# Kernel optimization log

Measured on AMD Instinct MI355X. Metric: run time of the kernel, lower is better.

The kernel has to match this reference:

```python
import jax, jax.numpy as jnp
import numpy as np
import math

B, S, D, H = 2, 2048, 512, 8  # batch, seq, d_hidden (= per-head dim here), n_heads


def _rope(x):
    # x: [B, H, S, D]; standard interleaved RoPE with base 10000
    b, h, s, d = x.shape
    inv_freq = 1.0 / (10000.0 ** (jnp.arange(0, d, 2, dtype=jnp.float32) / d))  # [d/2]
    ang = jnp.arange(s, dtype=jnp.float32)[:, None] * inv_freq[None, :]          # [S, d/2]
    cos, sin = jnp.cos(ang), jnp.sin(ang)
    x1, x2 = x[..., 0::2], x[..., 1::2]
    r1 = x1 * cos - x2 * sin
    r2 = x1 * sin + x2 * cos
    return jnp.stack([r1, r2], axis=-1).reshape(b, h, s, d).astype(x.dtype)


def setup_inputs() -> dict:
    key = jax.random.key(0)
    kq, k1, k2, k3, k4 = jax.random.split(key, 5)
    std = 0.02
    return {
        "q": jax.random.normal(kq, (B, S, D), dtype=jnp.float32),
        "W_q": jax.random.normal(k1, (H, D, D), dtype=jnp.float32) * std,
        "W_k": jax.random.normal(k2, (H, D, D), dtype=jnp.float32) * std,
        "W_v": jax.random.normal(k3, (H, D, D), dtype=jnp.float32) * std,
        "W_o": jax.random.normal(k4, (H * D, D), dtype=jnp.float32) * std,
    }


def reference(q, W_q, W_k, W_v, W_o):
    b, s, d = q.shape
    h = W_q.shape[0]
    scale = 1.0 / math.sqrt(d)
    qh = jnp.einsum('bsz,hzd->bhsd', q, W_q)
    kh = jnp.einsum('bsz,hzd->bhsd', q, W_k)
    vh = jnp.einsum('bsz,hzd->bhsd', q, W_v)
    qh = _rope(qh)
    kh = _rope(kh)
    scores = jnp.einsum('bhqd,bhkd->bhqk', qh, kh) * scale
    causal = jnp.triu(jnp.ones((s, s), dtype=bool), k=1)  # True above diagonal
    scores = jnp.where(causal, -jnp.inf, scores)
    probs = jax.nn.softmax(scores, axis=-1)  # dropout is identity in eval
    # NOTE: faithful to the original (transposed) einsum: contracts over the
    # query index z of probs with the sequence index z of v.
    out = jnp.einsum('bhzs,bhzd->bhsd', probs, vh)
    out = out.transpose(0, 2, 1, 3).reshape(b, s, h * d)
    return jnp.einsum('bsz,zd->bsd', out, W_o)
```

## Files before the change

kernel.cpp:

```cpp
#include <hip/hip_runtime.h>
#include <hip/hip_bf16.h>
#include <math.h>
#include <stdint.h>

#define BB 2
#define SS 2048
#define DD 512
#define HH 8
#define NTOK (BB*SS)
#define NQKV (3*HH*DD)
#define BHD  (HH*DD)
#define NBH  (BB*HH)
#define NTILE 136

typedef __attribute__((ext_vector_type(8))) short short8v;
typedef __attribute__((ext_vector_type(4))) float floatx4;

__device__ __forceinline__ unsigned short f2bf(float f) {
  unsigned int u = __builtin_bit_cast(unsigned int, f);
  u = (u + 0x7FFFu + ((u >> 16) & 1u)) >> 16;
  return (unsigned short)u;
}
__device__ __forceinline__ float bf2f(unsigned short s) {
  unsigned int u = ((unsigned int)s) << 16;
  return __builtin_bit_cast(float, u);
}
__device__ __forceinline__ void async16(const void* g, void* l) {
  __builtin_amdgcn_global_load_lds(
      (const __attribute__((address_space(1))) unsigned int*)g,
      (__attribute__((address_space(3))) unsigned int*)l, 16, 0, 0);
}

__global__ void k_convert_q(const float* __restrict__ q, unsigned short* __restrict__ qbf) {
  int i = (blockIdx.x * 256 + threadIdx.x) * 4;
  const float4 v = *(const float4*)&q[i];
  ushort4 o;
  o.x = f2bf(v.x); o.y = f2bf(v.y); o.z = f2bf(v.z); o.w = f2bf(v.w);
  *(ushort4*)&qbf[i] = o;
}

__global__ void k_rope_tab(float* __restrict__ rope) {
  const int idx = blockIdx.x * 256 + threadIdx.x;
  const int dp = idx >> 11, s = idx & 2047;
  const float inv = exp2f(-13.287712379549449f * (1.0f/256.0f) * (float)dp);
  float sn, cs;
  __sincosf((float)s * inv, &sn, &cs);
  rope[(size_t)idx * 2]     = cs;
  rope[(size_t)idx * 2 + 1] = sn;
}

__global__ void k_prep_w(const float* __restrict__ Wq, const float* __restrict__ Wk,
                         const float* __restrict__ Wv, const float* __restrict__ Wo,
                         unsigned short* __restrict__ Wcat, unsigned short* __restrict__ Wot) {
  __shared__ float t[32][33];
  const int z = blockIdx.z;
  const float* in; unsigned short* out; int inLD, outLD;
  float sc = 1.0f;
  if (z < 24) {
    int tsel = z / 8, h = z % 8;
    const float* w = (tsel == 0) ? Wq : (tsel == 1) ? Wk : Wv;
    if (tsel == 0) sc = 0.044194173824159216f;
    in = w + (size_t)h * DD * DD;
    out = Wcat + ((size_t)tsel * BHD + (size_t)h * DD) * DD;
    inLD = DD; outLD = DD;
  } else {
    int k = z - 24;
    in = Wo + (size_t)k * DD * DD;
    out = Wot + (size_t)k * DD;
    inLD = DD; outLD = BHD;
  }
  const int tx = threadIdx.x, ty = threadIdx.y;
  const int bx = blockIdx.x * 32, by = blockIdx.y * 32;
  for (int kk = 0; kk < 4; ++kk)
    t[ty + 8*kk][tx] = in[(size_t)(by + ty + 8*kk) * inLD + bx + tx];
  __syncthreads();
  for (int kk = 0; kk < 4; ++kk)
    out[(size_t)(bx + ty + 8*kk) * outLD + by + tx] = f2bf(t[tx][ty + 8*kk] * sc);
}

__global__ __launch_bounds__(256, 2)
void k_qkv(const unsigned short* __restrict__ Abf, const unsigned short* __restrict__ Bt,
           const float* __restrict__ rope,
           unsigned short* __restrict__ Qr, unsigned short* __restrict__ Kr,
           unsigned short* __restrict__ Vt) {
  __shared__ short As[128*32];
  __shared__ short Bs[256*32];
  const int tid = threadIdx.x;
  const int m0 = blockIdx.x * 128;
  const int n0 = blockIdx.y * 256;
  const int wave = tid >> 6, lane = tid & 63, qd = lane >> 4, c = lane & 15;
  const int wm = (wave >> 1) * 64, wn = (wave & 1) * 128;
  floatx4 acc[4][8] = {};
  const int e0 = tid * 8;
  const int r0 = e0 >> 5, c0 = e0 & 31;
  for (int k0 = 0; k0 < 512; k0 += 32) {
    __syncthreads();
    async16(&Abf[(size_t)(m0 + r0      ) * 512 + k0 + c0], &As[e0]);
    async16(&Abf[(size_t)(m0 + r0 +  64) * 512 + k0 + c0], &As[e0 + 2048]);
    async16(&Bt [(size_t)(n0 + r0      ) * 512 + k0 + c0], &Bs[e0]);
    async16(&Bt [(size_t)(n0 + r0 +  64) * 512 + k0 + c0], &Bs[e0 + 2048]);
    async16(&Bt [(size_t)(n0 + r0 + 128) * 512 + k0 + c0], &Bs[e0 + 4096]);
    async16(&Bt [(size_t)(n0 + r0 + 192) * 512 + k0 + c0], &Bs[e0 + 6144]);
    __syncthreads();
    short8v a[4], bfr[8];
    for (int mt = 0; mt < 4; ++mt) a[mt]   = *(const short8v*)&As[(wm + mt*16 + c)*32 + qd*8];
    for (int nt = 0; nt < 8; ++nt) bfr[nt] = *(const short8v*)&Bs[(wn + nt*16 + c)*32 + qd*8];
    for (int mt = 0; mt < 4; ++mt)
      for (int nt = 0; nt < 8; ++nt)
        acc[mt][nt] = __builtin_amdgcn_mfma_f32_16x16x32_bf16(a[mt], bfr[nt], acc[mt][nt], 0, 0, 0);
  }
  const int tsel = n0 >> 12;
  const int h = (n0 >> 9) & 7;
  const int bat = m0 >> 11;
  const int bh = bat * HH + h;
  const int dloc = (n0 & 511) + wn;
  if (tsel < 2) {
    unsigned short* dst = (tsel == 0) ? Qr : Kr;
    for (int nt = 0; nt < 8; ++nt) {
      const int d = dloc + nt*16 + c;
      const unsigned int sgn = (d & 1) ? 0u : 0x80000000u;
      const size_t rb = (size_t)(d >> 1) * (SS * 2);
      for (int mt = 0; mt < 4; ++mt) {
        const int mrow = (m0 & 2047) + wm + mt*16 + qd*4;
        const float4 t0 = *(const float4*)&rope[rb + (size_t)mrow * 2];
        const float4 t1 = *(const float4*)&rope[rb + (size_t)mrow * 2 + 4];
        const float cs[4] = {t0.x, t0.z, t1.x, t1.z};
        const float sn[4] = {t0.y, t0.w, t1.y, t1.w};
        for (int r = 0; r < 4; ++r) {
          const float v = acc[mt][nt][r];
          float p = __shfl_xor(v, 1, 64);
          p = __builtin_bit_cast(float, __builtin_bit_cast(unsigned int, p) ^ sgn);
          const float res = fmaf(p, sn[r], v * cs[r]);
          dst[((size_t)bh * SS + mrow + r) * DD + d] = f2bf(res);
        }
      }
    }
  } else {
    for (int nt = 0; nt < 8; ++nt) {
      const int d = dloc + nt*16 + c;
      const size_t vbase = ((size_t)bh * DD + d) * SS;
      for (int mt = 0; mt < 4; ++mt) {
        const int s = (m0 & 2047) + wm + mt*16 + qd*4;
        ushort4 u;
        u.x = f2bf(acc[mt][nt][0]); u.y = f2bf(acc[mt][nt][1]);
        u.z = f2bf(acc[mt][nt][2]); u.w = f2bf(acc[mt][nt][3]);
        *(ushort4*)&Vt[vbase + s] = u;
      }
    }
  }
}

__global__ __launch_bounds__(256)
void k_scores(const unsigned short* __restrict__ Qr, const unsigned short* __restrict__ Kr,
              unsigned short* __restrict__ Eg, float* __restrict__ lsum) {
  __shared__ short UN[17408];
  short* As0 = UN;
  short* As1 = UN + 4096;
  short* Bs0 = UN + 8192;
  short* Bs1 = UN + 12288;
  unsigned short* ET = (unsigned short*)UN;
  const int tid = threadIdx.x;
  const int bh = blockIdx.y;
  const int t = blockIdx.x;
  int zb = 0;
  while (((zb + 1) * (zb + 2)) / 2 <= t) ++zb;
  const int st = t - (zb * (zb + 1)) / 2;
  const int z0 = zb * 128, s0 = st * 128;
  const int wave = tid >> 6, lane = tid & 63, qd = lane >> 4, c = lane & 15;
  const int wm = (wave >> 1) * 64, wn = (wave & 1) * 64;
  const size_t qb = (size_t)bh * SS * DD;
  floatx4 acc[4][4] = {};
  const int e0 = tid * 8, e1 = e0 + 2048;
  const int r0 = e0 >> 5, c0 = e0 & 31, r1 = e1 >> 5, c1 = e1 & 31;
  for (int k0 = 0; k0 < 512; k0 += 64) {
    __syncthreads();
    async16(&Qr[qb + (size_t)(z0 + r0) * 512 + k0      + c0], &As0[e0]);
    async16(&Qr[qb + (size_t)(z0 + r1) * 512 + k0      + c1], &As0[e1]);
    async16(&Qr[qb + (size_t)(z0 + r0) * 512 + k0 + 32 + c0], &As1[e0]);
    async16(&Qr[qb + (size_t)(z0 + r1) * 512 + k0 + 32 + c1], &As1[e1]);
    async16(&Kr[qb + (size_t)(s0 + r0) * 512 + k0      + c0], &Bs0[e0]);
    async16(&Kr[qb + (size_t)(s0 + r1) * 512 + k0      + c1], &Bs0[e1]);
    async16(&Kr[qb + (size_t)(s0 + r0) * 512 + k0 + 32 + c0], &Bs1[e0]);
    async16(&Kr[qb + (size_t)(s0 + r1) * 512 + k0 + 32 + c1], &Bs1[e1]);
    __syncthreads();
    for (int kc = 0; kc < 2; ++kc) {
      const short* Asp = kc ? As1 : As0;
      const short* Bsp = kc ? Bs1 : Bs0;
      short8v a[4], bfr[4];
      for (int mt = 0; mt < 4; ++mt) a[mt]   = *(const short8v*)&Asp[(wm + mt*16 + c)*32 + qd*8];
      for (int nt = 0; nt < 4; ++nt) bfr[nt] = *(const short8v*)&Bsp[(wn + nt*16 + c)*32 + qd*8];
      for (int mt = 0; mt < 4; ++mt)
        for (int nt = 0; nt < 4; ++nt)
          acc[mt][nt] = __builtin_amdgcn_mfma_f32_16x16x32_bf16(a[mt], bfr[nt], acc[mt][nt], 0, 0, 0);
    }
  }
  const bool diag = (st == zb);
  for (int mt = 0; mt < 4; ++mt) {
    const int zl = wm + mt*16 + qd*4;
    float rs[4] = {0.f, 0.f, 0.f, 0.f};
    for (int nt = 0; nt < 4; ++nt) {
      const int sl = wn + nt*16 + c;
      for (int r = 0; r < 4; ++r) {
        float ev = __expf(acc[mt][nt][r]);
        if (diag && (sl > zl + r)) ev = 0.f;
        acc[mt][nt][r] = ev;
        rs[r] += ev;
      }
    }
    for (int off = 1; off < 16; off <<= 1)
      for (int r = 0; r < 4; ++r) rs[r] += __shfl_xor(rs[r], off, 64);
    if (c == 0)
      for (int r = 0; r < 4; ++r)
        atomicAdd(&lsum[(size_t)bh * SS + z0 + zl + r], rs[r]);
  }
  __syncthreads();
  for (int mt = 0; mt < 4; ++mt) {
    const int zl = wm + mt*16 + qd*4;
    for (int nt = 0; nt < 4; ++nt) {
      const int sl = wn + nt*16 + c;
      ushort4 u;
      u.x = f2bf(acc[mt][nt][0]); u.y = f2bf(acc[mt][nt][1]);
      u.z = f2bf(acc[mt][nt][2]); u.w = f2bf(acc[mt][nt][3]);
      *(ushort4*)&ET[sl * 136 + zl] = u;
    }
  }
  __syncthreads();
  const size_t tb = ((size_t)bh * NTILE + t) * 16384;
  for (int it = 0; it < 8; ++it) {
    const int e = it * 2048 + tid * 8;
    const int row = e >> 7, col = e & 127;
    *(short8v*)&Eg[tb + row * 128 + col] = *(const short8v*)&ET[row * 136 + col];
  }
}

__global__ void k_vscale(unsigned short* __restrict__ Vt, const float* __restrict__ lsum) {
  const int idx = (blockIdx.x * 256 + threadIdx.x) * 8;
  const int z = idx & (SS - 1);
  const int bh = idx >> 20;
  short8v v = *(const short8v*)&Vt[idx];
  const float* lp = &lsum[(size_t)bh * SS + z];
  short8v o;
  for (int i = 0; i < 8; ++i)
    o[i] = (short)f2bf(bf2f((unsigned short)v[i]) / lp[i]);
  *(short8v*)&Vt[idx] = o;
}

__global__ __launch_bounds__(256)
void k_pv(const unsigned short* __restrict__ Eg, const unsigned short* __restrict__ Vs,
          unsigned short* __restrict__ Ocat) {
  __shared__ short Vl[2][128*32];
  __shared__ short El[2][128*32];
  const int tid = threadIdx.x;
  const int d0 = blockIdx.x * 128;
  const int pr = blockIdx.y;
  const int bh = blockIdx.z;
  const int bat = bh >> 3, h = bh & 7;
  const int wave = tid >> 6, lane = tid & 63, qd = lane >> 4, c = lane & 15;
  const int wm = (wave >> 1) * 64, wn = (wave & 1) * 64;
  const size_t vbb = (size_t)bh * DD * SS;
  const int e = tid * 8;
  for (int sel = 0; sel < 2; ++sel) {
    const int st = sel ? (15 - pr) : pr;
    const int s0 = st * 128;
    floatx4 acc[4][4] = {};
    for (int zb = st; zb < 16; ++zb) {
      const size_t tb = ((size_t)bh * NTILE + (zb * (zb + 1)) / 2 + st) * 16384;
      for (int half = 0; half < 2; ++half) {
        const int zbase = zb * 128 + half * 64;
        __syncthreads();
        for (int i = 0; i < 4; ++i) {
          const int ee = e + i * 2048;
          const int kc = ee >> 12, row = (ee >> 5) & 127, col = ee & 31;
          async16(&Vs[vbb + (size_t)(d0 + row) * SS + zbase + kc * 32 + col], &Vl[kc][row * 32 + col]);
        }
        for (int i = 0; i < 4; ++i) {
          const int ee = e + i * 2048;
          const int kc = ee >> 12, row = (ee >> 5) & 127, col = ee & 31;
          async16(&Eg[tb + (size_t)row * 128 + half * 64 + kc * 32 + col], &El[kc][row * 32 + col]);
        }
        __syncthreads();
        for (int kc = 0; kc < 2; ++kc) {
          short8v a[4], b[4];
          for (int dt = 0; dt < 4; ++dt) a[dt] = *(const short8v*)&Vl[kc][(wm + dt*16 + c)*32 + qd*8];
          for (int nt = 0; nt < 4; ++nt) b[nt] = *(const short8v*)&El[kc][(wn + nt*16 + c)*32 + qd*8];
          for (int dt = 0; dt < 4; ++dt)
            for (int nt = 0; nt < 4; ++nt)
              acc[dt][nt] = __builtin_amdgcn_mfma_f32_16x16x32_bf16(a[dt], b[nt], acc[dt][nt], 0, 0, 0);
        }
      }
    }
    for (int nt = 0; nt < 4; ++nt) {
      const int sg = s0 + wn + nt*16 + c;
      const size_t ob = ((size_t)(bat * SS + sg)) * BHD + (size_t)h * DD + d0;
      for (int dt = 0; dt < 4; ++dt) {
        const int dloc = wm + dt*16 + qd*4;
        ushort4 u;
        u.x = f2bf(acc[dt][nt][0]); u.y = f2bf(acc[dt][nt][1]);
        u.z = f2bf(acc[dt][nt][2]); u.w = f2bf(acc[dt][nt][3]);
        *(ushort4*)&Ocat[ob + dloc] = u;
      }
    }
  }
}

__global__ __launch_bounds__(256)
void k_oproj(const unsigned short* __restrict__ Ocat, const unsigned short* __restrict__ Wot,
             float* __restrict__ out) {
  __shared__ short As[2][128*32];
  __shared__ short Bs[2][128*32];
  const int tid = threadIdx.x;
  const int m0 = blockIdx.x * 128;
  const int n0 = blockIdx.y * 128;
  const int ks = blockIdx.z * 1024;
  const int wave = tid >> 6, lane = tid & 63, qd = lane >> 4, c = lane & 15;
  const int wm = (wave >> 1) * 64, wn = (wave & 1) * 64;
  floatx4 acc[4][4] = {};
  const int e0 = tid * 8, e1 = e0 + 2048;
  const int r0 = e0 >> 5, c0 = e0 & 31, r1 = e1 >> 5, c1 = e1 & 31;
  for (int k0 = ks; k0 < ks + 1024; k0 += 64) {
    __syncthreads();
    for (int kc = 0; kc < 2; ++kc) {
      const int kk = k0 + kc * 32;
      async16(&Ocat[(size_t)(m0 + r0) * BHD + kk + c0], &As[kc][e0]);
      async16(&Ocat[(size_t)(m0 + r1) * BHD + kk + c1], &As[kc][e1]);
      async16(&Wot [(size_t)(n0 + r0) * BHD + kk + c0], &Bs[kc][e0]);
      async16(&Wot [(size_t)(n0 + r1) * BHD + kk + c1], &Bs[kc][e1]);
    }
    __syncthreads();
    for (int kc = 0; kc < 2; ++kc) {
      short8v a[4], b[4];
      for (int mt = 0; mt < 4; ++mt) a[mt] = *(const short8v*)&As[kc][(wm + mt*16 + c)*32 + qd*8];
      for (int nt = 0; nt < 4; ++nt) b[nt] = *(const short8v*)&Bs[kc][(wn + nt*16 + c)*32 + qd*8];
      for (int mt = 0; mt < 4; ++mt)
        for (int nt = 0; nt < 4; ++nt)
          acc[mt][nt] = __builtin_amdgcn_mfma_f32_16x16x32_bf16(a[mt], b[nt], acc[mt][nt], 0, 0, 0);
    }
  }
  for (int mt = 0; mt < 4; ++mt) {
    const int m = m0 + wm + mt*16 + qd*4;
    for (int nt = 0; nt < 4; ++nt) {
      const int n = n0 + wn + nt*16 + c;
      for (int r = 0; r < 4; ++r)
        atomicAdd(&out[(size_t)(m + r) * DD + n], acc[mt][nt][r]);
    }
  }
}

extern "C" void kernel_launch(void* const* d_in, const int* in_sizes, int n_in,
                              void* d_out, int out_size, void* d_ws, size_t ws_size,
                              hipStream_t stream) {
  const float* q  = (const float*)d_in[0];
  const float* Wq = (const float*)d_in[1];
  const float* Wk = (const float*)d_in[2];
  const float* Wv = (const float*)d_in[3];
  const float* Wo = (const float*)d_in[4];

  char* base = (char*)d_ws;
  unsigned short* Eg   = (unsigned short*)base;
  unsigned short* qbf  = (unsigned short*)base;
  unsigned short* Wcat = (unsigned short*)(base + 4194304);
  float*          rope = (float*)(base + 16777216);
  char* p = base + 71303168;
  unsigned short* Wot  = (unsigned short*)p; p += 4194304;
  unsigned short* Qr   = (unsigned short*)p;
  unsigned short* Ocat = (unsigned short*)p; p += 33554432;
  unsigned short* Kr   = (unsigned short*)p; p += 33554432;
  unsigned short* Vt   = (unsigned short*)p; p += 33554432;
  float*          lsum = (float*)p;

  hipMemsetAsync(lsum, 0, (size_t)NBH * SS * 4, stream);
  hipMemsetAsync(d_out, 0, (size_t)NTOK * DD * 4, stream);

  k_convert_q<<<NTOK*DD/1024, 256, 0, stream>>>(q, qbf);
  k_rope_tab<<<SS*256/256, 256, 0, stream>>>(rope);
  k_prep_w<<<dim3(16,16,32), dim3(32,8), 0, stream>>>(Wq, Wk, Wv, Wo, Wcat, Wot);
  k_qkv<<<dim3(32,48), 256, 0, stream>>>(qbf, Wcat, rope, Qr, Kr, Vt);
  k_scores<<<dim3(NTILE,16), 256, 0, stream>>>(Qr, Kr, Eg, lsum);
  k_vscale<<<NBH*DD*SS/(256*8), 256, 0, stream>>>(Vt, lsum);
  k_pv<<<dim3(4,8,16), 256, 0, stream>>>(Eg, Vt, Ocat);
  k_oproj<<<dim3(32,4,4), 256, 0, stream>>>(Ocat, Wot, (float*)d_out);
}
```

Baseline: 401.7 us.

## Double-buffer LDS tiles in all GEMM kernels and transpose the RoPE table

The QKV, scores, PV and output-projection kernels now keep two LDS buffers. Each loop step prefetches the next K-slice with async global-to-LDS loads while MFMA runs on the current slice, so each step needs one barrier instead of two. The point is to hide global load latency behind compute. The cost is twice the LDS per block, which could lower occupancy. Separately, the RoPE cos/sin table is stored position-major, and the QKV epilogue is reordered to read contiguous float2 pairs per row while writing rows of Q/K, for better locality in that epilogue.

```diff
diff --git a/kernel.cpp b/kernel.cpp
--- a/kernel.cpp
+++ b/kernel.cpp
@@ -41,7 +41,7 @@
 
 __global__ void k_rope_tab(float* __restrict__ rope) {
   const int idx = blockIdx.x * 256 + threadIdx.x;
-  const int dp = idx >> 11, s = idx & 2047;
+  const int s = idx >> 8, dp = idx & 255;
   const float inv = exp2f(-13.287712379549449f * (1.0f/256.0f) * (float)dp);
   float sn, cs;
   __sincosf((float)s * inv, &sn, &cs);
@@ -80,11 +80,11 @@
 
 __global__ __launch_bounds__(256, 2)
 void k_qkv(const unsigned short* __restrict__ Abf, const unsigned short* __restrict__ Bt,
-           const float* __restrict__ rope,
+           const float* __restrict__ ropeT,
            unsigned short* __restrict__ Qr, unsigned short* __restrict__ Kr,
            unsigned short* __restrict__ Vt) {
-  __shared__ short As[128*32];
-  __shared__ short Bs[256*32];
+  __shared__ short As[2][128*32];
+  __shared__ short Bs[2][256*32];
   const int tid = threadIdx.x;
   const int m0 = blockIdx.x * 128;
   const int n0 = blockIdx.y * 256;
@@ -93,21 +93,26 @@
   floatx4 acc[4][8] = {};
   const int e0 = tid * 8;
   const int r0 = e0 >> 5, c0 = e0 & 31;
+  auto STAGE = [&](int buf, int k0) {
+    async16(&Abf[(size_t)(m0 + r0      ) * 512 + k0 + c0], &As[buf][e0]);
+    async16(&Abf[(size_t)(m0 + r0 +  64) * 512 + k0 + c0], &As[buf][e0 + 2048]);
+    async16(&Bt [(size_t)(n0 + r0      ) * 512 + k0 + c0], &Bs[buf][e0]);
+    async16(&Bt [(size_t)(n0 + r0 +  64) * 512 + k0 + c0], &Bs[buf][e0 + 2048]);
+    async16(&Bt [(size_t)(n0 + r0 + 128) * 512 + k0 + c0], &Bs[buf][e0 + 4096]);
+    async16(&Bt [(size_t)(n0 + r0 + 192) * 512 + k0 + c0], &Bs[buf][e0 + 6144]);
+  };
+  STAGE(0, 0);
+  __syncthreads();
   for (int k0 = 0; k0 < 512; k0 += 32) {
-    __syncthreads();
-    async16(&Abf[(size_t)(m0 + r0      ) * 512 + k0 + c0], &As[e0]);
-    async16(&Abf[(size_t)(m0 + r0 +  64) * 512 + k0 + c0], &As[e0 + 2048]);
-    async16(&Bt [(size_t)(n0 + r0      ) * 512 + k0 + c0], &Bs[e0]);
-    async16(&Bt [(size_t)(n0 + r0 +  64) * 512 + k0 + c0], &Bs[e0 + 2048]);
-    async16(&Bt [(size_t)(n0 + r0 + 128) * 512 + k0 + c0], &Bs[e0 + 4096]);
-    async16(&Bt [(size_t)(n0 + r0 + 192) * 512 + k0 + c0], &Bs[e0 + 6144]);
-    __syncthreads();
+    const int cur = (k0 >> 5) & 1;
+    if (k0 < 480) STAGE(cur ^ 1, k0 + 32);
     short8v a[4], bfr[8];
-    for (int mt = 0; mt < 4; ++mt) a[mt]   = *(const short8v*)&As[(wm + mt*16 + c)*32 + qd*8];
-    for (int nt = 0; nt < 8; ++nt) bfr[nt] = *(const short8v*)&Bs[(wn + nt*16 + c)*32 + qd*8];
+    for (int mt = 0; mt < 4; ++mt) a[mt]   = *(const short8v*)&As[cur][(wm + mt*16 + c)*32 + qd*8];
+    for (int nt = 0; nt < 8; ++nt) bfr[nt] = *(const short8v*)&Bs[cur][(wn + nt*16 + c)*32 + qd*8];
     for (int mt = 0; mt < 4; ++mt)
       for (int nt = 0; nt < 8; ++nt)
         acc[mt][nt] = __builtin_amdgcn_mfma_f32_16x16x32_bf16(a[mt], bfr[nt], acc[mt][nt], 0, 0, 0);
+    __syncthreads();
   }
   const int tsel = n0 >> 12;
   const int h = (n0 >> 9) & 7;
@@ -116,22 +121,20 @@
   const int dloc = (n0 & 511) + wn;
   if (tsel < 2) {
     unsigned short* dst = (tsel == 0) ? Qr : Kr;
-    for (int nt = 0; nt < 8; ++nt) {
-      const int d = dloc + nt*16 + c;
-      const unsigned int sgn = (d & 1) ? 0u : 0x80000000u;
-      const size_t rb = (size_t)(d >> 1) * (SS * 2);
-      for (int mt = 0; mt < 4; ++mt) {
-        const int mrow = (m0 & 2047) + wm + mt*16 + qd*4;
-        const float4 t0 = *(const float4*)&rope[rb + (size_t)mrow * 2];
-        const float4 t1 = *(const float4*)&rope[rb + (size_t)mrow * 2 + 4];
-        const float cs[4] = {t0.x, t0.z, t1.x, t1.z};
-        const float sn[4] = {t0.y, t0.w, t1.y, t1.w};
-        for (int r = 0; r < 4; ++r) {
+    const int dp0 = (dloc >> 1) + (c >> 1);
+    const unsigned int sgn = (c & 1) ? 0u : 0x80000000u;
+    for (int mt = 0; mt < 4; ++mt) {
+      const int mrow = (m0 & 2047) + wm + mt*16 + qd*4;
+      for (int r = 0; r < 4; ++r) {
+        const int s = mrow + r;
+        const float2* rp = (const float2*)&ropeT[((size_t)s * 256 + dp0) * 2];
+        const size_t ob = ((size_t)bh * SS + s) * DD;
+        for (int nt = 0; nt < 8; ++nt) {
+          const float2 tt = rp[nt * 8];
           const float v = acc[mt][nt][r];
           float p = __shfl_xor(v, 1, 64);
           p = __builtin_bit_cast(float, __builtin_bit_cast(unsigned int, p) ^ sgn);
-          const float res = fmaf(p, sn[r], v * cs[r]);
-          dst[((size_t)bh * SS + mrow + r) * DD + d] = f2bf(res);
+          dst[ob + dloc + nt*16 + c] = f2bf(fmaf(p, tt.y, v * tt.x));
         }
       }
     }
@@ -154,10 +157,6 @@
 void k_scores(const unsigned short* __restrict__ Qr, const unsigned short* __restrict__ Kr,
               unsigned short* __restrict__ Eg, float* __restrict__ lsum) {
   __shared__ short UN[17408];
-  short* As0 = UN;
-  short* As1 = UN + 4096;
-  short* Bs0 = UN + 8192;
-  short* Bs1 = UN + 12288;
   unsigned short* ET = (unsigned short*)UN;
   const int tid = threadIdx.x;
   const int bh = blockIdx.y;
@@ -172,27 +171,28 @@
   floatx4 acc[4][4] = {};
   const int e0 = tid * 8, e1 = e0 + 2048;
   const int r0 = e0 >> 5, c0 = e0 & 31, r1 = e1 >> 5, c1 = e1 & 31;
-  for (int k0 = 0; k0 < 512; k0 += 64) {
+  auto STAGE = [&](int buf, int k0) {
+    short* A = UN + buf * 4096;
+    short* B = UN + 8192 + buf * 4096;
+    async16(&Qr[qb + (size_t)(z0 + r0) * 512 + k0 + c0], &A[e0]);
+    async16(&Qr[qb + (size_t)(z0 + r1) * 512 + k0 + c1], &A[e1]);
+    async16(&Kr[qb + (size_t)(s0 + r0) * 512 + k0 + c0], &B[e0]);
+    async16(&Kr[qb + (size_t)(s0 + r1) * 512 + k0 + c1], &B[e1]);
+  };
+  STAGE(0, 0);
+  __syncthreads();
+  for (int kk = 0; kk < 16; ++kk) {
+    const int cur = kk & 1;
+    if (kk < 15) STAGE(cur ^ 1, (kk + 1) * 32);
+    const short* Asp = UN + cur * 4096;
+    const short* Bsp = UN + 8192 + cur * 4096;
+    short8v a[4], bfr[4];
+    for (int mt = 0; mt < 4; ++mt) a[mt]   = *(const short8v*)&Asp[(wm + mt*16 + c)*32 + qd*8];
+    for (int nt = 0; nt < 4; ++nt) bfr[nt] = *(const short8v*)&Bsp[(wn + nt*16 + c)*32 + qd*8];
+    for (int mt = 0; mt < 4; ++mt)
+      for (int nt = 0; nt < 4; ++nt)
+        acc[mt][nt] = __builtin_amdgcn_mfma_f32_16x16x32_bf16(a[mt], bfr[nt], acc[mt][nt], 0, 0, 0);
     __syncthreads();
-    async16(&Qr[qb + (size_t)(z0 + r0) * 512 + k0      + c0], &As0[e0]);
-    async16(&Qr[qb + (size_t)(z0 + r1) * 512 + k0      + c1], &As0[e1]);
-    async16(&Qr[qb + (size_t)(z0 + r0) * 512 + k0 + 32 + c0], &As1[e0]);
-    async16(&Qr[qb + (size_t)(z0 + r1) * 512 + k0 + 32 + c1], &As1[e1]);
-    async16(&Kr[qb + (size_t)(s0 + r0) * 512 + k0      + c0], &Bs0[e0]);
-    async16(&Kr[qb + (size_t)(s0 + r1) * 512 + k0      + c1], &Bs0[e1]);
-    async16(&Kr[qb + (size_t)(s0 + r0) * 512 + k0 + 32 + c0], &Bs1[e0]);
-    async16(&Kr[qb + (size_t)(s0 + r1) * 512 + k0 + 32 + c1], &Bs1[e1]);
-    __syncthreads();
-    for (int kc = 0; kc < 2; ++kc) {
-      const short* Asp = kc ? As1 : As0;
-      const short* Bsp = kc ? Bs1 : Bs0;
-      short8v a[4], bfr[4];
-      for (int mt = 0; mt < 4; ++mt) a[mt]   = *(const short8v*)&Asp[(wm + mt*16 + c)*32 + qd*8];
-      for (int nt = 0; nt < 4; ++nt) bfr[nt] = *(const short8v*)&Bsp[(wn + nt*16 + c)*32 + qd*8];
-      for (int mt = 0; mt < 4; ++mt)
-        for (int nt = 0; nt < 4; ++nt)
-          acc[mt][nt] = __builtin_amdgcn_mfma_f32_16x16x32_bf16(a[mt], bfr[nt], acc[mt][nt], 0, 0, 0);
-    }
   }
   const bool diag = (st == zb);
   for (int mt = 0; mt < 4; ++mt) {
@@ -213,7 +213,6 @@
       for (int r = 0; r < 4; ++r)
         atomicAdd(&lsum[(size_t)bh * SS + z0 + zl + r], rs[r]);
   }
-  __syncthreads();
   for (int mt = 0; mt < 4; ++mt) {
     const int zl = wm + mt*16 + qd*4;
     for (int nt = 0; nt < 4; ++nt) {
@@ -248,8 +247,8 @@
 __global__ __launch_bounds__(256)
 void k_pv(const unsigned short* __restrict__ Eg, const unsigned short* __restrict__ Vs,
           unsigned short* __restrict__ Ocat) {
-  __shared__ short Vl[2][128*32];
-  __shared__ short El[2][128*32];
+  __shared__ short Vl[2][2][128*32];
+  __shared__ short El[2][2][128*32];
   const int tid = threadIdx.x;
   const int d0 = blockIdx.x * 128;
   const int pr = blockIdx.y;
@@ -259,35 +258,39 @@
   const int wm = (wave >> 1) * 64, wn = (wave & 1) * 64;
   const size_t vbb = (size_t)bh * DD * SS;
   const int e = tid * 8;
+  auto STAGE = [&](int buf, int zb, int half, int st) {
+    const size_t tb = ((size_t)bh * NTILE + (zb * (zb + 1)) / 2 + st) * 16384;
+    const int zbase = zb * 128 + half * 64;
+    for (int i = 0; i < 4; ++i) {
+      const int ee = e + i * 2048;
+      const int kc = ee >> 12, row = (ee >> 5) & 127, col = ee & 31;
+      async16(&Vs[vbb + (size_t)(d0 + row) * SS + zbase + kc * 32 + col], &Vl[buf][kc][row * 32 + col]);
+    }
+    for (int i = 0; i < 4; ++i) {
+      const int ee = e + i * 2048;
+      const int kc = ee >> 12, row = (ee >> 5) & 127, col = ee & 31;
+      async16(&Eg[tb + (size_t)row * 128 + half * 64 + kc * 32 + col], &El[buf][kc][row * 32 + col]);
+    }
+  };
   for (int sel = 0; sel < 2; ++sel) {
     const int st = sel ? (15 - pr) : pr;
     const int s0 = st * 128;
     floatx4 acc[4][4] = {};
-    for (int zb = st; zb < 16; ++zb) {
-      const size_t tb = ((size_t)bh * NTILE + (zb * (zb + 1)) / 2 + st) * 16384;
-      for (int half = 0; half < 2; ++half) {
-        const int zbase = zb * 128 + half * 64;
-        __syncthreads();
-        for (int i = 0; i < 4; ++i) {
-          const int ee = e + i * 2048;
-          const int kc = ee >> 12, row = (ee >> 5) & 127, col = ee & 31;
-          async16(&Vs[vbb + (size_t)(d0 + row) * SS + zbase + kc * 32 + col], &Vl[kc][row * 32 + col]);
-        }
-        for (int i = 0; i < 4; ++i) {
-          const int ee = e + i * 2048;
-          const int kc = ee >> 12, row = (ee >> 5) & 127, col = ee & 31;
-          async16(&Eg[tb + (size_t)row * 128 + half * 64 + kc * 32 + col], &El[kc][row * 32 + col]);
-        }
-        __syncthreads();
-        for (int kc = 0; kc < 2; ++kc) {
-          short8v a[4], b[4];
-          for (int dt = 0; dt < 4; ++dt) a[dt] = *(const short8v*)&Vl[kc][(wm + dt*16 + c)*32 + qd*8];
-          for (int nt = 0; nt < 4; ++nt) b[nt] = *(const short8v*)&El[kc][(wn + nt*16 + c)*32 + qd*8];
-          for (int dt = 0; dt < 4; ++dt)
-            for (int nt = 0; nt < 4; ++nt)
-              acc[dt][nt] = __builtin_amdgcn_mfma_f32_16x16x32_bf16(a[dt], b[nt], acc[dt][nt], 0, 0, 0);
-        }
-      }
+    const int nst = (16 - st) * 2;
+    STAGE(0, st, 0, st);
+    __syncthreads();
+    for (int q2 = 0; q2 < nst; ++q2) {
+      const int cur = q2 & 1;
+      if (q2 + 1 < nst) STAGE(cur ^ 1, st + ((q2 + 1) >> 1), (q2 + 1) & 1, st);
+      for (int kc = 0; kc < 2; ++kc) {
+        short8v a[4], b[4];
+        for (int dt = 0; dt < 4; ++dt) a[dt] = *(const short8v*)&Vl[cur][kc][(wm + dt*16 + c)*32 + qd*8];
+        for (int nt = 0; nt < 4; ++nt) b[nt] = *(const short8v*)&El[cur][kc][(wn + nt*16 + c)*32 + qd*8];
+        for (int dt = 0; dt < 4; ++dt)
+          for (int nt = 0; nt < 4; ++nt)
+            acc[dt][nt] = __builtin_amdgcn_mfma_f32_16x16x32_bf16(a[dt], b[nt], acc[dt][nt], 0, 0, 0);
+      }
+      __syncthreads();
     }
     for (int nt = 0; nt < 4; ++nt) {
       const int sg = s0 + wn + nt*16 + c;
@@ -306,8 +309,8 @@
 __global__ __launch_bounds__(256)
 void k_oproj(const unsigned short* __restrict__ Ocat, const unsigned short* __restrict__ Wot,
              float* __restrict__ out) {
-  __shared__ short As[2][128*32];
-  __shared__ short Bs[2][128*32];
+  __shared__ short As[2][2][128*32];
+  __shared__ short Bs[2][2][128*32];
   const int tid = threadIdx.x;
   const int m0 = blockIdx.x * 128;
   const int n0 = blockIdx.y * 128;
@@ -317,24 +320,29 @@
   floatx4 acc[4][4] = {};
   const int e0 = tid * 8, e1 = e0 + 2048;
   const int r0 = e0 >> 5, c0 = e0 & 31, r1 = e1 >> 5, c1 = e1 & 31;
-  for (int k0 = ks; k0 < ks + 1024; k0 += 64) {
-    __syncthreads();
+  auto STAGE = [&](int buf, int k0) {
     for (int kc = 0; kc < 2; ++kc) {
       const int kk = k0 + kc * 32;
-      async16(&Ocat[(size_t)(m0 + r0) * BHD + kk + c0], &As[kc][e0]);
-      async16(&Ocat[(size_t)(m0 + r1) * BHD + kk + c1], &As[kc][e1]);
-      async16(&Wot [(size_t)(n0 + r0) * BHD + kk + c0], &Bs[kc][e0]);
-      async16(&Wot [(size_t)(n0 + r1) * BHD + kk + c1], &Bs[kc][e1]);
-    }
-    __syncthreads();
+      async16(&Ocat[(size_t)(m0 + r0) * BHD + kk + c0], &As[buf][kc][e0]);
+      async16(&Ocat[(size_t)(m0 + r1) * BHD + kk + c1], &As[buf][kc][e1]);
+      async16(&Wot [(size_t)(n0 + r0) * BHD + kk + c0], &Bs[buf][kc][e0]);
+      async16(&Wot [(size_t)(n0 + r1) * BHD + kk + c1], &Bs[buf][kc][e1]);
+    }
+  };
+  STAGE(0, ks);
+  __syncthreads();
+  for (int t = 0; t < 16; ++t) {
+    const int cur = t & 1;
+    if (t < 15) STAGE(cur ^ 1, ks + (t + 1) * 64);
     for (int kc = 0; kc < 2; ++kc) {
       short8v a[4], b[4];
-      for (int mt = 0; mt < 4; ++mt) a[mt] = *(const short8v*)&As[kc][(wm + mt*16 + c)*32 + qd*8];
-      for (int nt = 0; nt < 4; ++nt) b[nt] = *(const short8v*)&Bs[kc][(wn + nt*16 + c)*32 + qd*8];
+      for (int mt = 0; mt < 4; ++mt) a[mt] = *(const short8v*)&As[cur][kc][(wm + mt*16 + c)*32 + qd*8];
+      for (int nt = 0; nt < 4; ++nt) b[nt] = *(const short8v*)&Bs[cur][kc][(wn + nt*16 + c)*32 + qd*8];
       for (int mt = 0; mt < 4; ++mt)
         for (int nt = 0; nt < 4; ++nt)
           acc[mt][nt] = __builtin_amdgcn_mfma_f32_16x16x32_bf16(a[mt], b[nt], acc[mt][nt], 0, 0, 0);
     }
+    __syncthreads();
   }
   for (int mt = 0; mt < 4; ++mt) {
     const int m = m0 + wm + mt*16 + qd*4;
```

Measured after the change: 407.3 us. About the same (+1.4%).
